# Kernel tuning notes

Hardware: AMD Instinct MI355X
Metric: run time of the kernel (lower is better)

Reference implementation:

```python
import jax, jax.numpy as jnp
import numpy as np

B, N, D, H, KS, DQ = 2048, 20, 512, 8, 3, 64
DK = D // H
LN_EPS = 1e-5


def _conv1d_same(x_bdn, w_oik):
    # x: [B, D, N], w: [O, I, K] -> [B, O, N], 'same' padding
    return jax.lax.conv_general_dilated(
        x_bdn, w_oik, window_strides=(1,), padding='SAME',
        dimension_numbers=('NCH', 'OIH', 'NCH'))


def _layernorm(x, g, b):
    m = jnp.mean(x, axis=-1, keepdims=True)
    v = jnp.var(x, axis=-1, keepdims=True)
    return (x - m) * jax.lax.rsqrt(v + LN_EPS) * g + b


def setup_inputs() -> dict:
    key = jax.random.key(0)
    ks = jax.random.split(key, 12)
    s = 0.02
    inp = {
        'x': jax.random.normal(ks[0], (B, N, D), dtype=jnp.float32),
        'Wq': jax.random.normal(ks[1], (D, D, KS), dtype=jnp.float32) * s,
        'Wk': jax.random.normal(ks[2], (D, D, KS), dtype=jnp.float32) * s,
        'Wv': jax.random.normal(ks[3], (D, D, KS), dtype=jnp.float32) * s,
        'gq_g': jnp.ones((D,), jnp.float32), 'gq_b': jnp.zeros((D,), jnp.float32),
        'gk_g': jnp.ones((D,), jnp.float32), 'gk_b': jnp.zeros((D,), jnp.float32),
        'gv_g': jnp.ones((D,), jnp.float32), 'gv_b': jnp.zeros((D,), jnp.float32),
        'rel_table': jax.random.normal(ks[4], (2 * N - 1, H), dtype=jnp.float32) * s,
        'gsb': jax.random.normal(ks[5], (H, N, N), dtype=jnp.float32) * s,
        'alpha': jnp.asarray(1.0, jnp.float32),
        'Wqf': jax.random.normal(ks[6], (D, DQ), dtype=jnp.float32) * s,
        'bqf': jnp.zeros((DQ,), jnp.float32),
        'Wqp': jax.random.normal(ks[7], (DQ, H), dtype=jnp.float32) * s,
        'bqp': jnp.zeros((H,), jnp.float32),
        'Wo': jax.random.normal(ks[8], (D, D), dtype=jnp.float32) * s,
        'bo': jnp.zeros((D,), jnp.float32),
    }
    return inp


def reference(x, Wq, Wk, Wv, gq_g, gq_b, gk_g, gk_b, gv_g, gv_b,
              rel_table, gsb, alpha, Wqf, bqf, Wqp, bqp, Wo, bo):
    xp = jnp.transpose(x, (0, 2, 1))  # [B, D, N]
    # conv QKV projections + LayerNorm + residual (use_conv_proj=True path)
    q = x + _layernorm(jnp.transpose(_conv1d_same(xp, Wq), (0, 2, 1)), gq_g, gq_b)
    k = x + _layernorm(jnp.transpose(_conv1d_same(xp, Wk), (0, 2, 1)), gk_g, gk_b)
    v = x + _layernorm(jnp.transpose(_conv1d_same(xp, Wv), (0, 2, 1)), gv_g, gv_b)
    # split heads: [B, H, N, DK]
    q = q.reshape(B, N, H, DK).transpose(0, 2, 1, 3)
    k = k.reshape(B, N, H, DK).transpose(0, 2, 1, 3)
    v = v.reshape(B, N, H, DK).transpose(0, 2, 1, 3)
    scale = 1.0 / jnp.sqrt(jnp.asarray(DK, jnp.float32))
    scores = jnp.einsum('bhnd,bhmd->bhnm', q, k) * scale  # [B, H, N, N]
    # relative positional bias over node index
    idx = jnp.arange(N)[:, None] - jnp.arange(N)[None, :] + N - 1  # [N, N]
    rel_bias = rel_table[idx]  # [N, N, H]
    scores = scores + jnp.transpose(rel_bias, (2, 0, 1))[None]
    # learned global spatial bias
    scores = scores + alpha * gsb[None]
    # dynamic adjacency bias from pairwise node features
    qf = jnp.tanh(x @ Wqf + bqf)  # [B, N, DQ]
    pair = qf[:, :, None, :] - qf[:, None, :, :]  # [B, N, N, DQ]
    dyn = pair @ Wqp + bqp  # [B, N, N, H]
    scores = scores + jnp.transpose(dyn, (0, 3, 1, 2))
    attn = jax.nn.softmax(scores, axis=-1)
    out = jnp.einsum('bhnm,bhmd->bhnd', attn, v)
    out = out.transpose(0, 2, 1, 3).reshape(B, N, D)
    return out @ Wo + bo
```

## Files before the change

kernel.cpp:

```cpp
#include <hip/hip_runtime.h>
#include <stdint.h>

#define Bn   2048
#define Nn   20
#define Dn   512
#define Hn   8
#define Mn   (Bn*Nn)
#define K3n  1536
#define NPn  22
#define BKn  32

typedef __attribute__((ext_vector_type(4))) float  floatx4;
typedef __attribute__((ext_vector_type(8))) __bf16 bf16x8;
typedef __attribute__((ext_vector_type(4))) __bf16 bf16x4;

__device__ __forceinline__ void gload_lds16(const void* g, void* l) {
  __builtin_amdgcn_global_load_lds(
      (const __attribute__((address_space(1))) void*)g,
      (__attribute__((address_space(3))) void*)l, 16, 0, 0);
}

__global__ void k_prep_xpad(const float* __restrict__ x, __bf16* __restrict__ xpad) {
  int idx = blockIdx.x * 256 + threadIdx.x;
  int d8 = idx & 63;
  int t  = idx >> 6;
  if (t >= Bn * NPn) return;
  int n = t % NPn;
  int b = t / NPn;
  bf16x8 v;
  if (n == 0 || n == NPn - 1) {
#pragma unroll
    for (int e = 0; e < 8; ++e) v[e] = (__bf16)0.f;
  } else {
    const float4 x0 = *(const float4*)(x + (size_t)((b * Nn + n - 1) * Dn) + d8 * 8);
    const float4 x1 = *(const float4*)(x + (size_t)((b * Nn + n - 1) * Dn) + d8 * 8 + 4);
    v[0] = (__bf16)x0.x; v[1] = (__bf16)x0.y; v[2] = (__bf16)x0.z; v[3] = (__bf16)x0.w;
    v[4] = (__bf16)x1.x; v[5] = (__bf16)x1.y; v[6] = (__bf16)x1.z; v[7] = (__bf16)x1.w;
  }
  *(bf16x8*)(xpad + (size_t)t * Dn + d8 * 8) = v;
}

__global__ void k_prep_wctf(const float* __restrict__ Wq, const float* __restrict__ Wk,
                            const float* __restrict__ Wv, __bf16* __restrict__ wctf) {
  int t = blockIdx.x * 256 + threadIdx.x;
  if (t >= 48 * 96 * 64) return;
  int l  = t & 63;
  int cb = (t >> 6) % 96;
  int kt = t / (96 * 64);
  int col = cb * 16 + (l & 15);
  int k   = kt * 32 + (l >> 4) * 8;
  int seg = col >> 9, o = col & 511;
  int kker = k >> 9, i = k & 511;
  const float* W = (seg == 0) ? Wq : ((seg == 1) ? Wk : Wv);
  const float* s = W + ((size_t)o * 512 + i) * 3 + kker;
  bf16x8 v;
#pragma unroll
  for (int e = 0; e < 8; ++e) v[e] = (__bf16)s[e * 3];
  *(bf16x8*)(wctf + (size_t)t * 8) = v;
}

__global__ void k_prep_wotf(const float* __restrict__ Wo, __bf16* __restrict__ wotf) {
  int t = blockIdx.x * 256 + threadIdx.x;
  if (t >= 16 * 32 * 64) return;
  int l  = t & 63;
  int cb = (t >> 6) & 31;
  int kt = t / (32 * 64);
  int col = cb * 16 + (l & 15);
  int k   = kt * 32 + (l >> 4) * 8;
  const float* s = Wo + (size_t)k * 512 + col;
  bf16x8 v;
#pragma unroll
  for (int e = 0; e < 8; ++e) v[e] = (__bf16)s[(size_t)e * 512];
  *(bf16x8*)(wotf + (size_t)t * 8) = v;
}

__global__ void k_prep_wqft(const float* __restrict__ Wqf, __bf16* __restrict__ wqft) {
  int idx = blockIdx.x * 256 + threadIdx.x;
  if (idx >= Dn * 64) return;
  int d = idx & 511, dq = idx >> 9;
  wqft[idx] = (__bf16)Wqf[d * 64 + dq];
}

__global__ void k_bias(const float* __restrict__ rel, const float* __restrict__ gsb,
                       const float* __restrict__ alpha, const float* __restrict__ bqp,
                       float* __restrict__ bias) {
  int idx = blockIdx.x * 256 + threadIdx.x;
  if (idx >= Hn * Nn * Nn) return;
  int j = idx % Nn;
  int i = (idx / Nn) % Nn;
  int h = idx / (Nn * Nn);
  bias[idx] = rel[(i - j + Nn - 1) * Hn + h] + alpha[0] * gsb[idx] + bqp[h];
}

#define LOADB4(DST, ADV) do {                                          \
    _Pragma("unroll")                                                  \
    for (int _tc = 0; _tc < 4; ++_tc)                                  \
      DST[_tc] = *(const bf16x8*)(gW + _tc * 512);                     \
    gW += (ADV);                                                       \
  } while (0)

#define QSTEP(CB, NB, CUR, NXT, DOSTAGE, ADV, VMS) do {                \
    if (DOSTAGE) {                                                     \
      gload_lds16(gA, lsA + (NB) * 4096 + dA); gA += BKn;              \
      LOADB4(NXT, ADV);                                                \
    }                                                                  \
    const __bf16* _L = lsA + (CB) * 4096;                              \
    bf16x8 _a0 = *(const bf16x8*)(_L + fAo[0]);                        \
    bf16x8 _a1 = *(const bf16x8*)(_L + fAo[1]);                        \
    bf16x8 _a2 = *(const bf16x8*)(_L + fAo[2]);                        \
    bf16x8 _a3 = *(const bf16x8*)(_L + fAo[3]);                        \
    bf16x8 _a4 = *(const bf16x8*)(_L + fAo[4]);                        \
    bf16x8 _a5 = *(const bf16x8*)(_L + fAo[5]);                        \
    bf16x8 _a6 = *(const bf16x8*)(_L + fAo[6]);                        \
    bf16x8 _a7 = *(const bf16x8*)(_L + fAo[7]);                        \
    __builtin_amdgcn_s_setprio(1);                                     \
    _Pragma("unroll")                                                  \
    for (int _tc = 0; _tc < 4; ++_tc) {                                \
      acc[0][_tc] = __builtin_amdgcn_mfma_f32_16x16x32_bf16(_a0, CUR[_tc], acc[0][_tc], 0, 0, 0); \
      acc[1][_tc] = __builtin_amdgcn_mfma_f32_16x16x32_bf16(_a1, CUR[_tc], acc[1][_tc], 0, 0, 0); \
      acc[2][_tc] = __builtin_amdgcn_mfma_f32_16x16x32_bf16(_a2, CUR[_tc], acc[2][_tc], 0, 0, 0); \
      acc[3][_tc] = __builtin_amdgcn_mfma_f32_16x16x32_bf16(_a3, CUR[_tc], acc[3][_tc], 0, 0, 0); \
      acc[4][_tc] = __builtin_amdgcn_mfma_f32_16x16x32_bf16(_a4, CUR[_tc], acc[4][_tc], 0, 0, 0); \
      acc[5][_tc] = __builtin_amdgcn_mfma_f32_16x16x32_bf16(_a5, CUR[_tc], acc[5][_tc], 0, 0, 0); \
      acc[6][_tc] = __builtin_amdgcn_mfma_f32_16x16x32_bf16(_a6, CUR[_tc], acc[6][_tc], 0, 0, 0); \
      acc[7][_tc] = __builtin_amdgcn_mfma_f32_16x16x32_bf16(_a7, CUR[_tc], acc[7][_tc], 0, 0, 0); \
    }                                                                  \
    __builtin_amdgcn_s_setprio(0);                                     \
    asm volatile("s_waitcnt vmcnt(" VMS ") lgkmcnt(0)\n\ts_barrier" ::: "memory"); \
  } while (0)

__global__ __launch_bounds__(512, 2)
void k_qkv(const __bf16* __restrict__ xpad, const __bf16* __restrict__ wctf,
           const float* __restrict__ gq_g, const float* __restrict__ gq_b,
           const float* __restrict__ gk_g, const float* __restrict__ gk_b,
           const float* __restrict__ gv_g, const float* __restrict__ gv_b,
           __bf16* __restrict__ qkv) {
  __shared__ __bf16 lsA[2 * 4096];

  const int tid  = threadIdx.x;
  const int wv   = tid >> 6;
  const int lane = tid & 63;
  const int quad = lane >> 4;
  const int l15  = lane & 15;

  const int bid   = blockIdx.x;
  const int xcd   = bid & 7;
  const int local = bid >> 3;
  const int seg   = local % 3;
  const int mt    = xcd * 40 + local / 3;
  const int m0    = mt * 128;

  const __bf16* gA;
  {
    int c   = tid;
    int row = c >> 2;
    int rk  = (c & 3) ^ ((row >> 1) & 3);
    int grow = m0 + row;
    int b = grow / Nn, n = grow - b * Nn;
    gA = xpad + (size_t)(b * NPn + n) * Dn + rk * 8;
  }
  const int dA = wv * 512;

  const __bf16* gW = wctf + ((size_t)(seg * 32 + wv * 4) * 512) + lane * 8;

  int fAo[8];
#pragma unroll
  for (int mi = 0; mi < 8; ++mi) {
    int row = mi * 16 + l15;
    fAo[mi] = row * BKn + (quad ^ ((row >> 1) & 3)) * 8;
  }

  floatx4 acc[8][4];
  const floatx4 zero = {0.f, 0.f, 0.f, 0.f};
#pragma unroll
  for (int i = 0; i < 8; ++i)
#pragma unroll
    for (int j = 0; j < 4; ++j) acc[i][j] = zero;

  bf16x8 bA[4], bB[4];

  gload_lds16(gA, lsA + dA); gA += BKn;
  LOADB4(bA, 49152);
  asm volatile("s_waitcnt vmcnt(0)\n\ts_barrier" ::: "memory");

#pragma unroll 1
  for (int it = 0; it < 23; ++it) {
    QSTEP(0, 1, bA, bB, true, 49152, "4");
    QSTEP(1, 0, bB, bA, true, 49152, "4");
  }
  QSTEP(0, 1, bA, bB, true,  49152, "4");
  QSTEP(1, 0, bB, bA, false, 49152, "0");

  float* red1 = (float*)lsA;
  float* red2 = red1 + 1024;
#pragma unroll
  for (int mi = 0; mi < 8; ++mi)
#pragma unroll
    for (int r = 0; r < 4; ++r) {
      float a = 0.f, b2 = 0.f;
#pragma unroll
      for (int tc = 0; tc < 4; ++tc) { float v = acc[mi][tc][r]; a += v; b2 += v * v; }
#pragma unroll
      for (int off = 1; off < 16; off <<= 1) {
        a  += __shfl_xor(a, off, 64);
        b2 += __shfl_xor(b2, off, 64);
      }
      if (l15 == 0) {
        int row = mi * 16 + quad * 4 + r;
        red1[row * 8 + wv] = a;
        red2[row * 8 + wv] = b2;
      }
    }
  __syncthreads();

  const float* gg = (seg == 0) ? gq_g : ((seg == 1) ? gk_g : gv_g);
  const float* bb = (seg == 0) ? gq_b : ((seg == 1) ? gk_b : gv_b);
#pragma unroll
  for (int mi = 0; mi < 8; ++mi)
#pragma unroll
    for (int r = 0; r < 4; ++r) {
      int row = mi * 16 + quad * 4 + r;
      float su = 0.f, sq = 0.f;
#pragma unroll
      for (int w = 0; w < 8; ++w) { su += red1[row * 8 + w]; sq += red2[row * 8 + w]; }
      float mn = su * (1.f / 512.f);
      float vv = sq * (1.f / 512.f) - mn * mn;
      float rstd = rsqrtf(vv + 1e-5f);
      int grow = m0 + row;
      int b = grow / Nn, n2 = grow - b * Nn;
      const __bf16* xr = xpad + (size_t)(b * NPn + n2 + 1) * Dn;
#pragma unroll
      for (int tc = 0; tc < 4; ++tc) {
        int col = wv * 64 + tc * 16 + l15;
        float val = (acc[mi][tc][r] - mn) * rstd * gg[col] + bb[col] + (float)xr[col];
        qkv[(size_t)grow * K3n + seg * 512 + col] = (__bf16)val;
      }
    }
}

__global__ __launch_bounds__(256)
void k_qfqp(const __bf16* __restrict__ xpad, const __bf16* __restrict__ wqft,
            const float* __restrict__ bqf, const float* __restrict__ wqp,
            float* __restrict__ qfp) {
  __shared__ __bf16 sA[64 * BKn];
  __shared__ __bf16 sB[64 * BKn];
  __shared__ float lWqpT[8 * 64];
  const int tid  = threadIdx.x;
  const int wave = tid >> 6;
  const int lane = tid & 63;
  const int quad = lane >> 4;
  const int l15  = lane & 15;
  const int m0   = blockIdx.x * 64;

#pragma unroll
  for (int t = tid; t < 512; t += 256) {
    int col = t & 63, h = t >> 6;
    lWqpT[t] = wqp[col * 8 + h];
  }

  int c = wave * 64 + lane;
  int rowc = c >> 2;
  int rk   = (c & 3) ^ ((rowc >> 1) & 3);
  int grow = m0 + rowc;
  int b = grow / Nn, n = grow - b * Nn;
  const __bf16* gA = xpad + (size_t)(b * NPn + n + 1) * Dn + rk * 8;
  const __bf16* gB = wqft + (size_t)rowc * Dn + rk * 8;

  int frow = wave * 16 + l15;
  const __bf16* fA = sA + frow * BKn + (quad ^ ((frow >> 1) & 3)) * 8;
  const __bf16* fB[4];
#pragma unroll
  for (int tc = 0; tc < 4; ++tc) {
    int col = tc * 16 + l15;
    fB[tc] = sB + col * BKn + (quad ^ ((col >> 1) & 3)) * 8;
  }

  const floatx4 zero = {0.f, 0.f, 0.f, 0.f};
  floatx4 acc[4] = {zero, zero, zero, zero};

  for (int kt = 0; kt < Dn / BKn; ++kt) {
    gload_lds16(gA, sA + wave * 512);
    gload_lds16(gB, sB + wave * 512);
    __syncthreads();
    bf16x8 a = *(const bf16x8*)fA;
#pragma unroll
    for (int tc = 0; tc < 4; ++tc)
      acc[tc] = __builtin_amdgcn_mfma_f32_16x16x32_bf16(a, *(const bf16x8*)fB[tc], acc[tc], 0, 0, 0);
    __syncthreads();
    gA += BKn; gB += BKn;
  }

  float part[4][8];
#pragma unroll
  for (int r = 0; r < 4; ++r)
#pragma unroll
    for (int h = 0; h < 8; ++h) part[r][h] = 0.f;
#pragma unroll
  for (int tc = 0; tc < 4; ++tc) {
    int col = tc * 16 + l15;
    float bq = bqf[col];
#pragma unroll
    for (int r = 0; r < 4; ++r) {
      float t = tanhf(acc[tc][r] + bq);
#pragma unroll
      for (int h = 0; h < 8; ++h) part[r][h] += t * lWqpT[h * 64 + col];
    }
  }
#pragma unroll
  for (int off = 1; off < 16; off <<= 1)
#pragma unroll
    for (int r = 0; r < 4; ++r)
#pragma unroll
      for (int h = 0; h < 8; ++h) part[r][h] += __shfl_xor(part[r][h], off, 64);
  if (l15 == 0) {
#pragma unroll
    for (int r = 0; r < 4; ++r) {
      int row = wave * 16 + quad * 4 + r;
#pragma unroll
      for (int h = 0; h < 8; ++h)
        qfp[(size_t)(m0 + row) * 8 + h] = part[r][h];
    }
  }
}

__global__ __launch_bounds__(256)
void k_attn(const __bf16* __restrict__ qkv, const float* __restrict__ qfp,
            const float* __restrict__ bias, __bf16* __restrict__ aout) {
  __shared__ float sq[4][Nn * 64];
  __shared__ float sk[4][Nn * 68];
  __shared__ float sv[4][Nn * 68];
  __shared__ float sp[4][Nn * Nn];
  __shared__ float sf[4][Nn];
  const int tid  = threadIdx.x;
  const int w    = tid >> 6;
  const int lane = tid & 63;
  const int p0 = blockIdx.x * 4 + w;
  const int b = p0 >> 3, h = p0 & 7;
  const __bf16* qb = qkv + (size_t)b * Nn * K3n + h * 64;

  for (int idx = lane; idx < 160; idx += 64) {
    int n = idx >> 3, c = (idx & 7) * 8;
    bf16x8 qv = *(const bf16x8*)(qb + (size_t)n * K3n + c);
    bf16x8 kv = *(const bf16x8*)(qb + (size_t)n * K3n + 512 + c);
    bf16x8 vv = *(const bf16x8*)(qb + (size_t)n * K3n + 1024 + c);
#pragma unroll
    for (int e = 0; e < 8; ++e) {
      sq[w][n * 64 + c + e] = (float)qv[e];
      sk[w][n * 68 + c + e] = (float)kv[e];
      sv[w][n * 68 + c + e] = (float)vv[e];
    }
  }
  if (lane < Nn) sf[w][lane] = qfp[(size_t)(b * Nn + lane) * 8 + h];
  __syncthreads();

  const float* bh = bias + h * Nn * Nn;
  for (int p = lane; p < Nn * Nn; p += 64) {
    int i = p / Nn, j = p - i * Nn;
    const float4* q4 = (const float4*)&sq[w][i * 64];
    const float4* k4 = (const float4*)&sk[w][j * 68];
    float s = 0.f;
#pragma unroll
    for (int d4 = 0; d4 < 16; ++d4) {
      float4 qa = q4[d4], ka = k4[d4];
      s += qa.x * ka.x + qa.y * ka.y + qa.z * ka.z + qa.w * ka.w;
    }
    sp[w][p] = s * 0.125f + bh[p] + sf[w][i] - sf[w][j];
  }
  __syncthreads();
  if (lane < Nn) {
    int i = lane;
    float* row = &sp[w][i * Nn];
    float mx = row[0];
    for (int j = 1; j < Nn; ++j) mx = fmaxf(mx, row[j]);
    float sum = 0.f;
    for (int j = 0; j < Nn; ++j) { float e = __expf(row[j] - mx); row[j] = e; sum += e; }
    float inv = 1.f / sum;
    for (int j = 0; j < Nn; ++j) row[j] *= inv;
  }
  __syncthreads();
  for (int i = 0; i < Nn; ++i) {
    float a = 0.f;
#pragma unroll
    for (int j = 0; j < Nn; ++j) a += sp[w][i * Nn + j] * sv[w][j * 68 + lane];
    aout[(size_t)(b * Nn + i) * Dn + h * 64 + lane] = (__bf16)a;
  }
}

__global__ __launch_bounds__(512, 2)
void k_oproj(const __bf16* __restrict__ aout, const __bf16* __restrict__ wotf,
             const float* __restrict__ bo, float* __restrict__ out) {
  __shared__ __bf16 lsA[2 * 4096];
  const int tid  = threadIdx.x;
  const int wv   = tid >> 6;
  const int lane = tid & 63;
  const int quad = lane >> 4;
  const int l15  = lane & 15;

  const int bid = blockIdx.x;
  const int m0  = ((bid & 7) * 40 + (bid >> 3)) * 128;

  const __bf16* gA;
  {
    int c   = tid;
    int row = c >> 2;
    int rk  = (c & 3) ^ ((row >> 1) & 3);
    gA = aout + (size_t)(m0 + row) * Dn + rk * 8;
  }
  const int dA = wv * 512;
  const __bf16* gW = wotf + ((size_t)(wv * 4) * 512) + lane * 8;

  int fAo[8];
#pragma unroll
  for (int mi = 0; mi < 8; ++mi) {
    int row = mi * 16 + l15;
    fAo[mi] = row * BKn + (quad ^ ((row >> 1) & 3)) * 8;
  }

  floatx4 acc[8][4];
  const floatx4 zero = {0.f, 0.f, 0.f, 0.f};
#pragma unroll
  for (int i = 0; i < 8; ++i)
#pragma unroll
    for (int j = 0; j < 4; ++j) acc[i][j] = zero;

  bf16x8 bA[4], bB[4];

  gload_lds16(gA, lsA + dA); gA += BKn;
  LOADB4(bA, 16384);
  asm volatile("s_waitcnt vmcnt(0)\n\ts_barrier" ::: "memory");

#pragma unroll 1
  for (int it = 0; it < 7; ++it) {
    QSTEP(0, 1, bA, bB, true, 16384, "4");
    QSTEP(1, 0, bB, bA, true, 16384, "4");
  }
  QSTEP(0, 1, bA, bB, true,  16384, "4");
  QSTEP(1, 0, bB, bA, false, 16384, "0");

#pragma unroll
  for (int mi = 0; mi < 8; ++mi)
#pragma unroll
    for (int r = 0; r < 4; ++r) {
      int row = mi * 16 + quad * 4 + r;
#pragma unroll
      for (int tc = 0; tc < 4; ++tc) {
        int col = wv * 64 + tc * 16 + l15;
        out[(size_t)(m0 + row) * Dn + col] = acc[mi][tc][r] + bo[col];
      }
    }
}

static const size_t OFF_XPAD = 0;
static const size_t OFF_WCT  = 46137344;
static const size_t OFF_WOT  = 50855936;
static const size_t OFF_WQFT = 51380224;
static const size_t OFF_QKV  = 51445760;
static const size_t OFF_QFP  = 177274880;
static const size_t OFF_BIAS = 178585600;
static const size_t OFF_AOUT = 0;

extern "C" void kernel_launch(void* const* d_in, const int* in_sizes, int n_in,
                              void* d_out, int out_size, void* d_ws, size_t ws_size,
                              hipStream_t stream) {
  (void)in_sizes; (void)n_in; (void)out_size; (void)ws_size;
  const float* x     = (const float*)d_in[0];
  const float* Wq    = (const float*)d_in[1];
  const float* Wk    = (const float*)d_in[2];
  const float* Wv    = (const float*)d_in[3];
  const float* gq_g  = (const float*)d_in[4];
  const float* gq_b  = (const float*)d_in[5];
  const float* gk_g  = (const float*)d_in[6];
  const float* gk_b  = (const float*)d_in[7];
  const float* gv_g  = (const float*)d_in[8];
  const float* gv_b  = (const float*)d_in[9];
  const float* rel   = (const float*)d_in[10];
  const float* gsb   = (const float*)d_in[11];
  const float* alpha = (const float*)d_in[12];
  const float* Wqf   = (const float*)d_in[13];
  const float* bqf   = (const float*)d_in[14];
  const float* Wqp   = (const float*)d_in[15];
  const float* bqp   = (const float*)d_in[16];
  const float* Wo    = (const float*)d_in[17];
  const float* bo    = (const float*)d_in[18];
  float* out = (float*)d_out;
  char* ws = (char*)d_ws;

  __bf16* xpad = (__bf16*)(ws + OFF_XPAD);
  __bf16* wctf = (__bf16*)(ws + OFF_WCT);
  __bf16* wotf = (__bf16*)(ws + OFF_WOT);
  __bf16* wqft = (__bf16*)(ws + OFF_WQFT);
  __bf16* qkv  = (__bf16*)(ws + OFF_QKV);
  float*  qfp  = (float*)(ws + OFF_QFP);
  float*  bias = (float*)(ws + OFF_BIAS);
  __bf16* aout = (__bf16*)(ws + OFF_AOUT);

  k_prep_xpad<<<(Bn * NPn * (Dn / 8) + 255) / 256, 256, 0, stream>>>(x, xpad);
  k_prep_wctf<<<(48 * 96 * 64 + 255) / 256, 256, 0, stream>>>(Wq, Wk, Wv, wctf);
  k_prep_wotf<<<(16 * 32 * 64 + 255) / 256, 256, 0, stream>>>(Wo, wotf);
  k_prep_wqft<<<(Dn * 64 + 255) / 256, 256, 0, stream>>>(Wqf, wqft);
  k_bias     <<<(Hn * Nn * Nn + 255) / 256, 256, 0, stream>>>(rel, gsb, alpha, bqp, bias);

  k_qkv <<<Mn / 128 * 3, 512, 0, stream>>>(xpad, wctf, gq_g, gq_b, gk_g, gk_b, gv_g, gv_b, qkv);
  k_qfqp<<<Mn / 64, 256, 0, stream>>>(xpad, wqft, bqf, Wqp, qfp);
  k_attn<<<(Bn * Hn) / 4, 256, 0, stream>>>(qkv, qfp, bias, aout);
  k_oproj<<<Mn / 128, 512, 0, stream>>>(aout, wotf, bo, out);
}
```

Measured before the change: 571.3 us.

## Fuse output projection into attention kernel and merge small prep kernels

The attention kernel now runs one 512-thread block per batch element, one wave per head. Each block writes its attention output as bf16 into shared memory, then does the Wo projection with MFMA directly from there and writes the final fp32 output. This removes the global aout write/read round trip and the separate o-projection launch. V is also kept as bf16 in shared memory, and the Wo/Wqf/bias prep kernels are folded into one launch to cut launch overhead. In exchange, every block re-streams the whole Wo weight through cache. The 20-row tiles pad to 32 MFMA rows, and about 123 KB of shared memory per block limits occupancy.

```diff
diff --git a/kernel.cpp b/kernel.cpp
--- a/kernel.cpp
+++ b/kernel.cpp
@@ -59,37 +59,35 @@
   *(bf16x8*)(wctf + (size_t)t * 8) = v;
 }
 
-__global__ void k_prep_wotf(const float* __restrict__ Wo, __bf16* __restrict__ wotf) {
-  int t = blockIdx.x * 256 + threadIdx.x;
-  if (t >= 16 * 32 * 64) return;
-  int l  = t & 63;
-  int cb = (t >> 6) & 31;
-  int kt = t / (32 * 64);
-  int col = cb * 16 + (l & 15);
-  int k   = kt * 32 + (l >> 4) * 8;
-  const float* s = Wo + (size_t)k * 512 + col;
-  bf16x8 v;
-#pragma unroll
-  for (int e = 0; e < 8; ++e) v[e] = (__bf16)s[(size_t)e * 512];
-  *(bf16x8*)(wotf + (size_t)t * 8) = v;
-}
-
-__global__ void k_prep_wqft(const float* __restrict__ Wqf, __bf16* __restrict__ wqft) {
+__global__ void k_prep_misc(const float* __restrict__ Wo, __bf16* __restrict__ wotf,
+                            const float* __restrict__ Wqf, __bf16* __restrict__ wqft,
+                            const float* __restrict__ rel, const float* __restrict__ gsb,
+                            const float* __restrict__ alpha, const float* __restrict__ bqp,
+                            float* __restrict__ bias) {
   int idx = blockIdx.x * 256 + threadIdx.x;
-  if (idx >= Dn * 64) return;
-  int d = idx & 511, dq = idx >> 9;
-  wqft[idx] = (__bf16)Wqf[d * 64 + dq];
-}
-
-__global__ void k_bias(const float* __restrict__ rel, const float* __restrict__ gsb,
-                       const float* __restrict__ alpha, const float* __restrict__ bqp,
-                       float* __restrict__ bias) {
-  int idx = blockIdx.x * 256 + threadIdx.x;
-  if (idx >= Hn * Nn * Nn) return;
-  int j = idx % Nn;
-  int i = (idx / Nn) % Nn;
-  int h = idx / (Nn * Nn);
-  bias[idx] = rel[(i - j + Nn - 1) * Hn + h] + alpha[0] * gsb[idx] + bqp[h];
+  if (idx < 16 * 32 * 64) {
+    int t = idx;
+    int l  = t & 63;
+    int cb = (t >> 6) & 31;
+    int kt = t / (32 * 64);
+    int col = cb * 16 + (l & 15);
+    int k   = kt * 32 + (l >> 4) * 8;
+    const float* s = Wo + (size_t)k * 512 + col;
+    bf16x8 v;
+#pragma unroll
+    for (int e = 0; e < 8; ++e) v[e] = (__bf16)s[(size_t)e * 512];
+    *(bf16x8*)(wotf + (size_t)t * 8) = v;
+  } else if (idx < 65536) {
+    int t = idx - 32768;
+    int d = t & 511, dq = t >> 9;
+    wqft[t] = (__bf16)Wqf[d * 64 + dq];
+  } else if (idx < 65536 + Hn * Nn * Nn) {
+    int t = idx - 65536;
+    int j = t % Nn;
+    int i = (t / Nn) % Nn;
+    int h = t / (Nn * Nn);
+    bias[t] = rel[(i - j + Nn - 1) * Hn + h] + alpha[0] * gsb[t] + bqp[h];
+  }
 }
 
 #define LOADB4(DST, ADV) do {                                          \
@@ -323,19 +321,32 @@
   }
 }
 
-__global__ __launch_bounds__(256)
+__global__ __launch_bounds__(512)
 void k_attn(const __bf16* __restrict__ qkv, const float* __restrict__ qfp,
-            const float* __restrict__ bias, __bf16* __restrict__ aout) {
-  __shared__ float sq[4][Nn * 64];
-  __shared__ float sk[4][Nn * 68];
-  __shared__ float sv[4][Nn * 68];
-  __shared__ float sp[4][Nn * Nn];
-  __shared__ float sf[4][Nn];
+            const float* __restrict__ bias, const __bf16* __restrict__ wotf,
+            const float* __restrict__ bo, float* __restrict__ out) {
+  __shared__ float sm[30880];
+  float*  sq  = sm;
+  float*  sk  = sm + 10240;
+  __bf16* svb = (__bf16*)(sm + 21120);
+  float*  sp  = sm + 27520;
+  float*  sf  = sm + 30720;
+  __bf16* sA  = (__bf16*)sm;
+
   const int tid  = threadIdx.x;
-  const int w    = tid >> 6;
+  const int wv   = tid >> 6;
   const int lane = tid & 63;
-  const int p0 = blockIdx.x * 4 + w;
-  const int b = p0 >> 3, h = p0 & 7;
+  const int quad = lane >> 4;
+  const int l15  = lane & 15;
+  const int b    = blockIdx.x;
+  const int h    = wv;
+
+  float*  wsq = sq  + wv * 1280;
+  float*  wsk = sk  + wv * 1360;
+  __bf16* wsv = svb + wv * 1600;
+  float*  wsp = sp  + wv * 400;
+  float*  wsf = sf  + wv * 20;
+
   const __bf16* qb = qkv + (size_t)b * Nn * K3n + h * 64;
 
   for (int idx = lane; idx < 160; idx += 64) {
@@ -345,31 +356,31 @@
     bf16x8 vv = *(const bf16x8*)(qb + (size_t)n * K3n + 1024 + c);
 #pragma unroll
     for (int e = 0; e < 8; ++e) {
-      sq[w][n * 64 + c + e] = (float)qv[e];
-      sk[w][n * 68 + c + e] = (float)kv[e];
-      sv[w][n * 68 + c + e] = (float)vv[e];
-    }
-  }
-  if (lane < Nn) sf[w][lane] = qfp[(size_t)(b * Nn + lane) * 8 + h];
+      wsq[n * 64 + c + e] = (float)qv[e];
+      wsk[n * 68 + c + e] = (float)kv[e];
+    }
+    *(bf16x8*)(wsv + n * 80 + c) = vv;
+  }
+  if (lane < Nn) wsf[lane] = qfp[(size_t)(b * Nn + lane) * 8 + h];
   __syncthreads();
 
   const float* bh = bias + h * Nn * Nn;
   for (int p = lane; p < Nn * Nn; p += 64) {
     int i = p / Nn, j = p - i * Nn;
-    const float4* q4 = (const float4*)&sq[w][i * 64];
-    const float4* k4 = (const float4*)&sk[w][j * 68];
+    const float4* q4 = (const float4*)&wsq[i * 64];
+    const float4* k4 = (const float4*)&wsk[j * 68];
     float s = 0.f;
 #pragma unroll
     for (int d4 = 0; d4 < 16; ++d4) {
       float4 qa = q4[d4], ka = k4[d4];
       s += qa.x * ka.x + qa.y * ka.y + qa.z * ka.z + qa.w * ka.w;
     }
-    sp[w][p] = s * 0.125f + bh[p] + sf[w][i] - sf[w][j];
+    wsp[p] = s * 0.125f + bh[p] + wsf[i] - wsf[j];
   }
   __syncthreads();
   if (lane < Nn) {
     int i = lane;
-    float* row = &sp[w][i * Nn];
+    float* row = &wsp[i * Nn];
     float mx = row[0];
     for (int j = 1; j < Nn; ++j) mx = fmaxf(mx, row[j]);
     float sum = 0.f;
@@ -381,73 +392,70 @@
   for (int i = 0; i < Nn; ++i) {
     float a = 0.f;
 #pragma unroll
-    for (int j = 0; j < Nn; ++j) a += sp[w][i * Nn + j] * sv[w][j * 68 + lane];
-    aout[(size_t)(b * Nn + i) * Dn + h * 64 + lane] = (__bf16)a;
-  }
-}
-
-__global__ __launch_bounds__(512, 2)
-void k_oproj(const __bf16* __restrict__ aout, const __bf16* __restrict__ wotf,
-             const float* __restrict__ bo, float* __restrict__ out) {
-  __shared__ __bf16 lsA[2 * 4096];
-  const int tid  = threadIdx.x;
-  const int wv   = tid >> 6;
-  const int lane = tid & 63;
-  const int quad = lane >> 4;
-  const int l15  = lane & 15;
-
-  const int bid = blockIdx.x;
-  const int m0  = ((bid & 7) * 40 + (bid >> 3)) * 128;
-
-  const __bf16* gA;
-  {
-    int c   = tid;
-    int row = c >> 2;
-    int rk  = (c & 3) ^ ((row >> 1) & 3);
-    gA = aout + (size_t)(m0 + row) * Dn + rk * 8;
-  }
-  const int dA = wv * 512;
+    for (int j = 0; j < Nn; ++j) a += wsp[i * Nn + j] * (float)wsv[j * 80 + lane];
+    sA[i * 520 + wv * 64 + lane] = (__bf16)a;
+  }
+  __syncthreads();
+
   const __bf16* gW = wotf + ((size_t)(wv * 4) * 512) + lane * 8;
-
-  int fAo[8];
-#pragma unroll
-  for (int mi = 0; mi < 8; ++mi) {
-    int row = mi * 16 + l15;
-    fAo[mi] = row * BKn + (quad ^ ((row >> 1) & 3)) * 8;
-  }
-
-  floatx4 acc[8][4];
   const floatx4 zero = {0.f, 0.f, 0.f, 0.f};
-#pragma unroll
-  for (int i = 0; i < 8; ++i)
-#pragma unroll
-    for (int j = 0; j < 4; ++j) acc[i][j] = zero;
-
+  floatx4 acc0[4] = {zero, zero, zero, zero};
+  floatx4 acc1[4] = {zero, zero, zero, zero};
   bf16x8 bA[4], bB[4];
-
-  gload_lds16(gA, lsA + dA); gA += BKn;
-  LOADB4(bA, 16384);
-  asm volatile("s_waitcnt vmcnt(0)\n\ts_barrier" ::: "memory");
+#pragma unroll
+  for (int tc = 0; tc < 4; ++tc) bA[tc] = *(const bf16x8*)(gW + tc * 512);
+  gW += 16384;
 
 #pragma unroll 1
-  for (int it = 0; it < 7; ++it) {
-    QSTEP(0, 1, bA, bB, true, 16384, "4");
-    QSTEP(1, 0, bB, bA, true, 16384, "4");
-  }
-  QSTEP(0, 1, bA, bB, true,  16384, "4");
-  QSTEP(1, 0, bB, bA, false, 16384, "0");
-
-#pragma unroll
-  for (int mi = 0; mi < 8; ++mi)
-#pragma unroll
-    for (int r = 0; r < 4; ++r) {
-      int row = mi * 16 + quad * 4 + r;
+  for (int it = 0; it < 8; ++it) {
+    const int kt0 = 2 * it, kt1 = 2 * it + 1;
+#pragma unroll
+    for (int tc = 0; tc < 4; ++tc) bB[tc] = *(const bf16x8*)(gW + tc * 512);
+    gW += 16384;
+    {
+      bf16x8 a0 = *(const bf16x8*)(sA + (size_t)l15 * 520 + kt0 * 32 + quad * 8);
+      bf16x8 a1 = *(const bf16x8*)(sA + (size_t)(16 + l15) * 520 + kt0 * 32 + quad * 8);
+#pragma unroll
+      for (int tc = 0; tc < 4; ++tc) {
+        acc0[tc] = __builtin_amdgcn_mfma_f32_16x16x32_bf16(a0, bA[tc], acc0[tc], 0, 0, 0);
+        acc1[tc] = __builtin_amdgcn_mfma_f32_16x16x32_bf16(a1, bA[tc], acc1[tc], 0, 0, 0);
+      }
+    }
+    if (it < 7) {
+#pragma unroll
+      for (int tc = 0; tc < 4; ++tc) bA[tc] = *(const bf16x8*)(gW + tc * 512);
+      gW += 16384;
+    }
+    {
+      bf16x8 a0 = *(const bf16x8*)(sA + (size_t)l15 * 520 + kt1 * 32 + quad * 8);
+      bf16x8 a1 = *(const bf16x8*)(sA + (size_t)(16 + l15) * 520 + kt1 * 32 + quad * 8);
+#pragma unroll
+      for (int tc = 0; tc < 4; ++tc) {
+        acc0[tc] = __builtin_amdgcn_mfma_f32_16x16x32_bf16(a0, bB[tc], acc0[tc], 0, 0, 0);
+        acc1[tc] = __builtin_amdgcn_mfma_f32_16x16x32_bf16(a1, bB[tc], acc1[tc], 0, 0, 0);
+      }
+    }
+  }
+
+#pragma unroll
+  for (int r = 0; r < 4; ++r) {
+    int row0 = quad * 4 + r;
+    float* o0 = out + (size_t)(b * Nn + row0) * Dn;
+#pragma unroll
+    for (int tc = 0; tc < 4; ++tc) {
+      int col = wv * 64 + tc * 16 + l15;
+      o0[col] = acc0[tc][r] + bo[col];
+    }
+    if (quad == 0) {
+      int row1 = 16 + r;
+      float* o1 = out + (size_t)(b * Nn + row1) * Dn;
 #pragma unroll
       for (int tc = 0; tc < 4; ++tc) {
         int col = wv * 64 + tc * 16 + l15;
-        out[(size_t)(m0 + row) * Dn + col] = acc[mi][tc][r] + bo[col];
+        o1[col] = acc1[tc][r] + bo[col];
       }
     }
+  }
 }
 
 static const size_t OFF_XPAD = 0;
@@ -457,7 +465,6 @@
 static const size_t OFF_QKV  = 51445760;
 static const size_t OFF_QFP  = 177274880;
 static const size_t OFF_BIAS = 178585600;
-static const size_t OFF_AOUT = 0;
 
 extern "C" void kernel_launch(void* const* d_in, const int* in_sizes, int n_in,
                               void* d_out, int out_size, void* d_ws, size_t ws_size,
@@ -492,16 +499,13 @@
   __bf16* qkv  = (__bf16*)(ws + OFF_QKV);
   float*  qfp  = (float*)(ws + OFF_QFP);
   float*  bias = (float*)(ws + OFF_BIAS);
-  __bf16* aout = (__bf16*)(ws + OFF_AOUT);
 
   k_prep_xpad<<<(Bn * NPn * (Dn / 8) + 255) / 256, 256, 0, stream>>>(x, xpad);
   k_prep_wctf<<<(48 * 96 * 64 + 255) / 256, 256, 0, stream>>>(Wq, Wk, Wv, wctf);
-  k_prep_wotf<<<(16 * 32 * 64 + 255) / 256, 256, 0, stream>>>(Wo, wotf);
-  k_prep_wqft<<<(Dn * 64 + 255) / 256, 256, 0, stream>>>(Wqf, wqft);
-  k_bias     <<<(Hn * Nn * Nn + 255) / 256, 256, 0, stream>>>(rel, gsb, alpha, bqp, bias);
+  k_prep_misc<<<(65536 + Hn * Nn * Nn + 255) / 256, 256, 0, stream>>>(
+      Wo, wotf, Wqf, wqft, rel, gsb, alpha, bqp, bias);
 
   k_qkv <<<Mn / 128 * 3, 512, 0, stream>>>(xpad, wctf, gq_g, gq_b, gk_g, gk_b, gv_g, gv_b, qkv);
   k_qfqp<<<Mn / 64, 256, 0, stream>>>(xpad, wqft, bqf, Wqp, qfp);
-  k_attn<<<(Bn * Hn) / 4, 256, 0, stream>>>(qkv, qfp, bias, aout);
-  k_oproj<<<Mn / 128, 512, 0, stream>>>(aout, wotf, bo, out);
-}
+  k_attn<<<Bn, 512, 0, stream>>>(qkv, qfp, bias, wotf, bo, out);
+}
```

New measurement: 580.2 us. About the same (+1.6%).
